# Optimization experiments

Measured on AMD Instinct MI355X. Metric: run time of the kernel, lower is better.

## Reference

```python
import jax, jax.numpy as jnp
import numpy as np

B, N, HIDDEN = 4, 2048, 512
N_HEADS, HEAD_DIM = 8, 64
N_CANCER = 32
SCALE = float(np.sqrt(HEAD_DIM))


def setup_inputs() -> dict:
    key = jax.random.key(0)
    ks = jax.random.split(key, 16)
    s = 0.02
    return {
        "x": jax.random.normal(ks[0], (B, N, HIDDEN), dtype=jnp.float32),
        "cancer_type": jax.random.randint(ks[1], (B,), 0, N_CANCER, dtype=jnp.int64),
        "attn_mask": jnp.zeros((B, N), dtype=bool),
        "wq": jax.random.normal(ks[2], (HIDDEN, HIDDEN), dtype=jnp.float32) * s,
        "bq": jnp.zeros((HIDDEN,), dtype=jnp.float32),
        "wk": jax.random.normal(ks[3], (HIDDEN, HIDDEN), dtype=jnp.float32) * s,
        "bk": jnp.zeros((HIDDEN,), dtype=jnp.float32),
        "wv": jax.random.normal(ks[4], (HIDDEN, HIDDEN), dtype=jnp.float32) * s,
        "bv": jnp.zeros((HIDDEN,), dtype=jnp.float32),
        "wo": jax.random.normal(ks[5], (HIDDEN, HIDDEN), dtype=jnp.float32) * s,
        "bo": jnp.zeros((HIDDEN,), dtype=jnp.float32),
        "bias_emb": jax.random.normal(ks[6], (N_CANCER, N_HEADS), dtype=jnp.float32) * s,
        "keymod_emb": jax.random.normal(ks[7], (N_CANCER, HIDDEN), dtype=jnp.float32) * s,
    }


def reference(x, cancer_type, attn_mask, wq, bq, wk, bk, wv, bv, wo, bo, bias_emb, keymod_emb):
    Bc, Nc, _ = x.shape
    # projections (torch Linear: x @ W.T + b), split heads -> (B, H, N, D)
    def split_heads(t):
        return t.reshape(Bc, Nc, N_HEADS, HEAD_DIM).transpose(0, 2, 1, 3)
    q = split_heads(x @ wq.T + bq)
    k = split_heads(x @ wk.T + bk)
    v = split_heads(x @ wv.T + bv)
    # cancer-conditioned key offset: (B, H, 1, D)
    ct_key = keymod_emb[cancer_type].reshape(Bc, 1, N_HEADS, HEAD_DIM).transpose(0, 2, 1, 3)
    k = k + ct_key
    # scores + per-head cancer bias
    attn = jnp.einsum("bhnd,bhmd->bhnm", q, k) / SCALE
    ct_bias = bias_emb[cancer_type]  # (B, H)
    attn = attn + ct_bias[:, :, None, None]
    attn = jnp.where(attn_mask[:, None, None, :], -jnp.inf, attn)
    attn = jax.nn.softmax(attn, axis=-1)
    # dropout is identity in eval mode
    out = jnp.einsum("bhnm,bhmd->bhnd", attn, v)
    out = out.transpose(0, 2, 1, 3).reshape(Bc, Nc, HIDDEN)
    return out @ wo.T + bo
```

## Files before the change

### kernel.cpp

```cpp
#include <hip/hip_runtime.h>

#define B_    4
#define N_    2048
#define HID   512
#define NH    8
#define HD    64
#define TOK   (B_ * N_)
#define LOG2E 1.4426950408889634f

typedef __attribute__((ext_vector_type(8))) short short8;
typedef __attribute__((ext_vector_type(4))) float f32x4;
typedef unsigned short u16;

static __device__ __forceinline__ u16 f2bf(float f) {
    unsigned int u = __builtin_bit_cast(unsigned int, f);
    u += 0x7FFFu + ((u >> 16) & 1u);
    return (u16)(u >> 16);
}
static __device__ __forceinline__ float bf2f(u16 v) {
    return __builtin_bit_cast(float, (unsigned)v << 16);
}
static __device__ __forceinline__ unsigned pktrunc(float a, float b) {
    return __builtin_amdgcn_perm(__builtin_bit_cast(unsigned, b),
                                 __builtin_bit_cast(unsigned, a), 0x07060302u);
}

static __device__ __forceinline__ void dma16(const void* g, void* l) {
    __builtin_amdgcn_global_load_lds(
        (const __attribute__((address_space(1))) unsigned int*)(unsigned long long)g,
        (__attribute__((address_space(3))) unsigned int*)(unsigned int)(unsigned long long)l,
        16, 0, 0);
}

__global__ __launch_bounds__(256) void cvt_all(
    const float* __restrict__ x,
    const float* __restrict__ w0, const float* __restrict__ w1,
    const float* __restrict__ w2, const float* __restrict__ w3,
    u16* __restrict__ xb,
    u16* __restrict__ d0, u16* __restrict__ d1,
    u16* __restrict__ d2, u16* __restrict__ d3)
{
    const int bid = blockIdx.x;
    const float* s;
    u16* d;
    int off;
    if (bid < 4096) { s = x; d = xb; off = bid; }
    else {
        const int t = (bid - 4096) >> 8;
        off = (bid - 4096) & 255;
        s = t == 0 ? w0 : t == 1 ? w1 : t == 2 ? w2 : w3;
        d = t == 0 ? d0 : t == 1 ? d1 : t == 2 ? d2 : d3;
    }
    const int i = off * 1024 + threadIdx.x * 4;
    const float4 v = *(const float4*)&s[i];
    ushort4 o;
    o.x = f2bf(v.x); o.y = f2bf(v.y); o.z = f2bf(v.z); o.w = f2bf(v.w);
    *(ushort4*)&d[i] = o;
}

__global__ __launch_bounds__(256) void gemm_qkv(
    const u16* __restrict__ xb,
    const u16* __restrict__ W0, const u16* __restrict__ W1, const u16* __restrict__ W2,
    const float* __restrict__ bias0, const float* __restrict__ bias1, const float* __restrict__ bias2,
    u16* __restrict__ Qg, u16* __restrict__ Kg, u16* __restrict__ Vtg)
{
    const int z = blockIdx.z;
    const u16*   Wz   = z == 0 ? W0 : z == 1 ? W1 : W2;
    const float* bias = z == 0 ? bias0 : z == 1 ? bias1 : bias2;

    const u16* Ap; const u16* Bp; int arow0, brow0;
    if (z < 2) { Ap = Wz; Bp = xb; arow0 = blockIdx.y * 128; brow0 = blockIdx.x * 128; }
    else       { Ap = xb; Bp = Wz; arow0 = blockIdx.x * 128; brow0 = blockIdx.y * 128; }

    __shared__ u16 ABs[2][2][128 * 32];

    const int tid  = threadIdx.x;
    const int w    = tid >> 6, lane = tid & 63;
    const int wr   = w >> 1, wc = w & 1;
    const int t16  = lane & 15, q4 = lane >> 4;

    const int dmr  = lane >> 2;
    const int dmc8 = (lane & 3) ^ ((lane >> 2) & 3) ^ ((lane >> 4) & 3);

    f32x4 acc[4][4];
    #pragma unroll
    for (int mt = 0; mt < 4; ++mt)
        #pragma unroll
        for (int nt = 0; nt < 4; ++nt)
            acc[mt][nt] = (f32x4){0.f, 0.f, 0.f, 0.f};

    #define QKV_DMA(p, k0)                                                      \
        _Pragma("unroll")                                                       \
        for (int i = 0; i < 2; ++i) {                                           \
            const int c = w * 2 + i;                                            \
            dma16(&Ap[(size_t)(arow0 + c * 16 + dmr) * HID + (k0) + dmc8 * 8],  \
                  &ABs[p][0][c * 512]);                                         \
            dma16(&Bp[(size_t)(brow0 + c * 16 + dmr) * HID + (k0) + dmc8 * 8],  \
                  &ABs[p][1][c * 512]);                                         \
        }

    QKV_DMA(0, 0)

    const int swz = (t16 ^ (t16 >> 2)) & 3;

    for (int it = 0; it < HID / 32; ++it) {
        __syncthreads();
        if (it + 1 < HID / 32) { QKV_DMA((it + 1) & 1, (it + 1) * 32) }

        const int p = it & 1;
        short8 af[4], bf[4];
        #pragma unroll
        for (int mt = 0; mt < 4; ++mt)
            af[mt] = *(const short8*)&ABs[p][0][(wr * 64 + mt * 16 + t16) * 32 + (q4 ^ swz) * 8];
        #pragma unroll
        for (int nt = 0; nt < 4; ++nt)
            bf[nt] = *(const short8*)&ABs[p][1][(wc * 64 + nt * 16 + t16) * 32 + (q4 ^ swz) * 8];
        #pragma unroll
        for (int mt = 0; mt < 4; ++mt)
            #pragma unroll
            for (int nt = 0; nt < 4; ++nt)
                acc[mt][nt] = __builtin_amdgcn_mfma_f32_16x16x32_bf16(
                    af[mt], bf[nt], acc[mt][nt], 0, 0, 0);
    }

    if (z < 2) {
        const float qs = (z == 0) ? 0.125f * LOG2E : 1.0f;
        u16* Cg = (z == 0) ? Qg : Kg;
        u16 (*St)[72] = (u16(*)[72])&ABs[0][0][0];
        #pragma unroll
        for (int p = 0; p < 2; ++p) {
            __syncthreads();
            if (wr == p) {
                #pragma unroll
                for (int mt = 0; mt < 4; ++mt) {
                    const f32x4 bv = *(const f32x4*)&bias[arow0 + p * 64 + mt * 16 + q4 * 4];
                    #pragma unroll
                    for (int nt = 0; nt < 4; ++nt) {
                        const int np = wc * 64 + nt * 16 + t16;
                        uint2 pk;
                        pk.x = pktrunc((acc[mt][nt][0] + bv[0]) * qs,
                                       (acc[mt][nt][1] + bv[1]) * qs);
                        pk.y = pktrunc((acc[mt][nt][2] + bv[2]) * qs,
                                       (acc[mt][nt][3] + bv[3]) * qs);
                        *(uint2*)&St[np][mt * 16 + q4 * 4] = pk;
                    }
                }
            }
            __syncthreads();
            const int h = blockIdx.y * 2 + p;
            #pragma unroll
            for (int it = 0; it < 4; ++it) {
                const int task = tid + it * 256;
                const int np = task >> 3, ch = task & 7;
                const int nf = brow0 + np;
                const int b = nf >> 11, n = nf & (N_ - 1);
                *(short8*)&Cg[(((size_t)(b * NH + h)) * N_ + n) * HD + ch * 8] =
                    *(const short8*)&St[np][ch * 8];
            }
        }
    } else {
        u16 (*St)[72] = (u16(*)[72])&ABs[0][0][0];
        const int b = arow0 >> 11;
        #pragma unroll
        for (int p = 0; p < 2; ++p) {
            __syncthreads();
            if (wr == p) {
                #pragma unroll
                for (int nt = 0; nt < 4; ++nt) {
                    const int jp = wc * 64 + nt * 16 + t16;
                    const float bv = bias[brow0 + jp];
                    #pragma unroll
                    for (int mt = 0; mt < 4; ++mt) {
                        uint2 pk;
                        pk.x = pktrunc(acc[mt][nt][0] + bv, acc[mt][nt][1] + bv);
                        pk.y = pktrunc(acc[mt][nt][2] + bv, acc[mt][nt][3] + bv);
                        *(uint2*)&St[jp][mt * 16 + q4 * 4] = pk;
                    }
                }
            }
            __syncthreads();
            const int nb = (arow0 & (N_ - 1)) + p * 64;
            #pragma unroll
            for (int it = 0; it < 2; ++it) {
                const int task = tid + it * 256;
                const int jp = task >> 2, qc = task & 3;
                u16 v[16];
                #pragma unroll
                for (int e = 0; e < 16; ++e) {
                    const int np = qc * 16 + e;
                    const int n  = ((np & 3) << 4) | (np >> 2);
                    v[e] = St[jp][n];
                }
                const int j = brow0 + jp, h = j >> 6, d = j & 63;
                u16* dst = &Vtg[(((size_t)(b * NH + h)) * HD + d) * N_ + nb + qc * 16];
                *(short8*)(dst)     = *(const short8*)&v[0];
                *(short8*)(dst + 8) = *(const short8*)&v[8];
            }
        }
    }
}

__global__ __launch_bounds__(256) void gemm_o(
    const u16* __restrict__ A, const u16* __restrict__ W,
    const float* __restrict__ bias, float* __restrict__ C)
{
    __shared__ u16 ABs[2][(64 + 128) * 32];

    const int tid  = threadIdx.x;
    const int row0 = blockIdx.x * 64, col0 = blockIdx.y * 128;
    const int w    = tid >> 6, lane = tid & 63;
    const int wr   = w >> 1, wc = w & 1;
    const int t16  = lane & 15, q4 = lane >> 4;

    const int dmr  = lane >> 2;
    const int dmc8 = (lane & 3) ^ ((lane >> 2) & 3) ^ ((lane >> 4) & 3);

    f32x4 acc[2][4];
    #pragma unroll
    for (int mt = 0; mt < 2; ++mt)
        #pragma unroll
        for (int nt = 0; nt < 4; ++nt)
            acc[mt][nt] = (f32x4){0.f, 0.f, 0.f, 0.f};

    #define O_DMA(p, k0)                                                        \
        dma16(&A[(size_t)(row0 + w * 16 + dmr) * HID + (k0) + dmc8 * 8],        \
              &ABs[p][w * 512]);                                                \
        _Pragma("unroll")                                                       \
        for (int i = 0; i < 2; ++i) {                                           \
            const int c = w * 2 + i;                                            \
            dma16(&W[(size_t)(col0 + c * 16 + dmr) * HID + (k0) + dmc8 * 8],    \
                  &ABs[p][2048 + c * 512]);                                     \
        }

    O_DMA(0, 0)

    const int swz = (t16 ^ (t16 >> 2)) & 3;

    for (int it = 0; it < HID / 32; ++it) {
        __syncthreads();
        if (it + 1 < HID / 32) { O_DMA((it + 1) & 1, (it + 1) * 32) }

        const int p = it & 1;
        short8 af[2], bf[4];
        #pragma unroll
        for (int mt = 0; mt < 2; ++mt)
            af[mt] = *(const short8*)&ABs[p][(wr * 32 + mt * 16 + t16) * 32 + (q4 ^ swz) * 8];
        #pragma unroll
        for (int nt = 0; nt < 4; ++nt)
            bf[nt] = *(const short8*)&ABs[p][2048 + (wc * 64 + nt * 16 + t16) * 32 + (q4 ^ swz) * 8];
        #pragma unroll
        for (int mt = 0; mt < 2; ++mt)
            #pragma unroll
            for (int nt = 0; nt < 4; ++nt)
                acc[mt][nt] = __builtin_amdgcn_mfma_f32_16x16x32_bf16(
                    af[mt], bf[nt], acc[mt][nt], 0, 0, 0);
    }

    #pragma unroll
    for (int nt = 0; nt < 4; ++nt) {
        const int j = col0 + wc * 64 + nt * 16 + t16;
        const float bv = bias[j];
        #pragma unroll
        for (int mt = 0; mt < 2; ++mt)
            #pragma unroll
            for (int r = 0; r < 4; ++r) {
                const int i = row0 + wr * 32 + mt * 16 + q4 * 4 + r;
                C[(size_t)i * HID + j] = acc[mt][nt][r] + bv;
            }
    }
}

__global__ __launch_bounds__(256) void flash_mfma(
    const u16* __restrict__ Qg, const u16* __restrict__ Kg,
    const u16* __restrict__ Vtg, const unsigned char* __restrict__ msk,
    u16* __restrict__ Op, float* __restrict__ Lp)
{
    __shared__ u16 KVs[2][2][64 * 64];
    __shared__ u16 Ps[4][32][72];
    __shared__ unsigned Mnd[16][32];

    const int tid = threadIdx.x;
    const int w = tid >> 6, lane = tid & 63;
    const int t16 = lane & 15, q4 = lane >> 4;
    const int bh = blockIdx.y, b = bh >> 3;
    const int z = blockIdx.z;
    const int kofs = z * (N_ / 2);
    const int qrow0 = blockIdx.x * 128;
    const int qbase = qrow0 + w * 32;

    const size_t hb = (size_t)bh * N_ * HD;
    const u16* Qh  = Qg + hb;
    const u16* Kh  = Kg + hb;
    const u16* Vth = Vtg + hb;
    const unsigned char* mrow = msk + b * N_;

    #pragma unroll
    for (int it = 0; it < 2; ++it) {
        const int e = tid + it * 256;
        const int kt = e >> 5, sl = e & 31;
        const int tt = sl >> 1, wd = sl & 1;
        const int k0 = kofs + kt * 64 + wd * 32 + tt;
        const unsigned lo = mrow[k0]      ? 0u : 0x0000FFFFu;
        const unsigned hi = mrow[k0 + 16] ? 0u : 0xFFFF0000u;
        Mnd[kt][sl] = lo | hi;
    }

    short8 qf[2][2];
    #pragma unroll
    for (int mt = 0; mt < 2; ++mt)
        #pragma unroll
        for (int kk = 0; kk < 2; ++kk)
            qf[mt][kk] = *(const short8*)
                &Qh[(size_t)(qbase + mt * 16 + t16) * HD + kk * 32 + q4 * 8];

    const short8 ones8 = {0x3F80, 0x3F80, 0x3F80, 0x3F80,
                          0x3F80, 0x3F80, 0x3F80, 0x3F80};

    f32x4 o[2][4], ls[2];
    #pragma unroll
    for (int mt = 0; mt < 2; ++mt) {
        #pragma unroll
        for (int nt = 0; nt < 4; ++nt) o[mt][nt] = (f32x4){0.f, 0.f, 0.f, 0.f};
        ls[mt] = (f32x4){0.f, 0.f, 0.f, 0.f};
    }

    const int dmr  = lane >> 3;
    const int dmc8 = (lane & 7) ^ ((lane >> 3) & 7);

    #define FLASH_DMA(p, kb)                                                    \
        _Pragma("unroll")                                                       \
        for (int i = 0; i < 2; ++i) {                                           \
            const int c = w * 2 + i;                                            \
            dma16(&Kh[(size_t)((kb) + c * 8 + dmr) * HD + dmc8 * 8],            \
                  &KVs[p][0][c * 512]);                                         \
            dma16(&Vth[(size_t)(c * 8 + dmr) * N_ + (kb) + dmc8 * 8],           \
                  &KVs[p][1][c * 512]);                                         \
        }

    FLASH_DMA(0, kofs)

    const int swz7 = t16 & 7;

    for (int kt = 0; kt < 16; ++kt) {
        __syncthreads();
        if (kt + 1 < 16) { FLASH_DMA((kt + 1) & 1, kofs + (kt + 1) * 64) }
        const int p = kt & 1;

        f32x4 s[2][4];
        #pragma unroll
        for (int mt = 0; mt < 2; ++mt)
            #pragma unroll
            for (int f = 0; f < 4; ++f)
                s[mt][f] = (f32x4){0.f, 0.f, 0.f, 0.f};
        #pragma unroll
        for (int f = 0; f < 4; ++f) {
            #pragma unroll
            for (int kk = 0; kk < 2; ++kk) {
                const short8 kf = *(const short8*)
                    &KVs[p][0][(f * 16 + t16) * 64 + ((kk * 4 + q4) ^ swz7) * 8];
                #pragma unroll
                for (int mt = 0; mt < 2; ++mt)
                    s[mt][f] = __builtin_amdgcn_mfma_f32_16x16x32_bf16(
                        qf[mt][kk], kf, s[mt][f], 0, 0, 0);
            }
        }

        const uint2 mnd = *(const uint2*)&Mnd[kt][t16 * 2];

        #pragma unroll
        for (int mt = 0; mt < 2; ++mt) {
            #pragma unroll
            for (int r = 0; r < 4; ++r) {
                const float e0 = __builtin_amdgcn_exp2f(s[mt][0][r]);
                const float e1 = __builtin_amdgcn_exp2f(s[mt][1][r]);
                const float e2 = __builtin_amdgcn_exp2f(s[mt][2][r]);
                const float e3 = __builtin_amdgcn_exp2f(s[mt][3][r]);
                uint2 pk;
                pk.x = pktrunc(e0, e1) & mnd.x;
                pk.y = pktrunc(e2, e3) & mnd.y;
                *(uint2*)&Ps[w][mt * 16 + q4 * 4 + r][t16 * 4] = pk;
            }
        }

        short8 pf[2][2];
        #pragma unroll
        for (int mt = 0; mt < 2; ++mt)
            #pragma unroll
            for (int kk = 0; kk < 2; ++kk)
                pf[mt][kk] = *(const short8*)&Ps[w][mt * 16 + t16][kk * 32 + q4 * 8];
        #pragma unroll
        for (int mt = 0; mt < 2; ++mt)
            #pragma unroll
            for (int kk = 0; kk < 2; ++kk)
                ls[mt] = __builtin_amdgcn_mfma_f32_16x16x32_bf16(
                    pf[mt][kk], ones8, ls[mt], 0, 0, 0);
        #pragma unroll
        for (int nt = 0; nt < 4; ++nt) {
            #pragma unroll
            for (int kk = 0; kk < 2; ++kk) {
                const short8 vf = *(const short8*)
                    &KVs[p][1][(nt * 16 + t16) * 64 + ((kk * 4 + q4) ^ swz7) * 8];
                #pragma unroll
                for (int mt = 0; mt < 2; ++mt)
                    o[mt][nt] = __builtin_amdgcn_mfma_f32_16x16x32_bf16(
                        pf[mt][kk], vf, o[mt][nt], 0, 0, 0);
            }
        }
    }

    const size_t obase = (((size_t)z * 32 + bh)) * N_ * HD;
    #pragma unroll
    for (int mt = 0; mt < 2; ++mt) {
        #pragma unroll
        for (int r = 0; r < 4; ++r) {
            const int n = qbase + mt * 16 + q4 * 4 + r;
            if (t16 == 0) Lp[((size_t)z * 32 + bh) * N_ + n] = ls[mt][r];
            #pragma unroll
            for (int nt = 0; nt < 4; ++nt)
                Op[obase + (size_t)n * HD + nt * 16 + t16] = f2bf(o[mt][nt][r]);
        }
    }
}

__global__ __launch_bounds__(256) void reduce_o(
    const u16* __restrict__ Op, const float* __restrict__ Lp,
    u16* __restrict__ AOg)
{
    const int e = blockIdx.x * 256 + threadIdx.x;
    const int d4 = e & 15;
    const int n  = (e >> 4) & (N_ - 1);
    const int bh = e >> 15;
    const size_t base = (((size_t)bh) * N_ + n) * HD + d4 * 4;
    const ushort4 a = *(const ushort4*)&Op[base];
    const ushort4 c = *(const ushort4*)&Op[(size_t)32 * N_ * HD + base];
    const float inv = 1.f / (Lp[(size_t)bh * N_ + n] + Lp[(size_t)(32 + bh) * N_ + n]);
    ushort4 o;
    o.x = f2bf((bf2f(a.x) + bf2f(c.x)) * inv);
    o.y = f2bf((bf2f(a.y) + bf2f(c.y)) * inv);
    o.z = f2bf((bf2f(a.z) + bf2f(c.z)) * inv);
    o.w = f2bf((bf2f(a.w) + bf2f(c.w)) * inv);
    const int b = bh >> 3, h = bh & 7;
    *(ushort4*)&AOg[(((size_t)b * N_ + n)) * HID + h * 64 + d4 * 4] = o;
}

extern "C" void kernel_launch(void* const* d_in, const int* in_sizes, int n_in,
                              void* d_out, int out_size, void* d_ws, size_t ws_size,
                              hipStream_t stream) {
    const float* x  = (const float*)d_in[0];
    const unsigned char* mask = (const unsigned char*)d_in[2];
    const float* wq = (const float*)d_in[3];
    const float* bq = (const float*)d_in[4];
    const float* wk = (const float*)d_in[5];
    const float* bk = (const float*)d_in[6];
    const float* wv = (const float*)d_in[7];
    const float* bv = (const float*)d_in[8];
    const float* wo = (const float*)d_in[9];
    const float* bo = (const float*)d_in[10];

    char* ws = (char*)d_ws;
    u16* xb  = (u16*)(ws);
    u16* wqb = (u16*)(ws + (8u << 20));
    u16* wkb = (u16*)(ws + (8u << 20) + (512u << 10));
    u16* wvb = (u16*)(ws + (8u << 20) + (1024u << 10));
    u16* wob = (u16*)(ws + (8u << 20) + (1536u << 10));
    u16* Qg  = (u16*)(ws + (10u << 20));
    u16* Kg  = (u16*)(ws + (18u << 20));
    u16* Vtg = (u16*)(ws + (26u << 20));
    u16* Op  = (u16*)(ws + (34u << 20));
    float* Lp = (float*)(ws + (50u << 20));
    u16* AOg = xb;

    cvt_all<<<5120, 256, 0, stream>>>(x, wq, wk, wv, wo, xb, wqb, wkb, wvb, wob);

    gemm_qkv<<<dim3(TOK / 128, HID / 128, 3), 256, 0, stream>>>(
        xb, wqb, wkb, wvb, bq, bk, bv, Qg, Kg, Vtg);

    flash_mfma<<<dim3(N_ / 128, B_ * NH, 2), 256, 0, stream>>>(
        Qg, Kg, Vtg, mask, Op, Lp);

    reduce_o<<<(32 * N_ * 16) / 256, 256, 0, stream>>>(Op, Lp, AOg);

    gemm_o<<<dim3(TOK / 64, HID / 128), 256, 0, stream>>>(
        AOg, wob, bo, (float*)d_out);
}
```

Baseline: 179.3 us.

## Fuse split-softmax reduction into output projection GEMM and unroll double-buffer loops

Removes the separate reduce_o kernel and instead has the output-projection GEMM load both flash-attention partial outputs plus their row sums, combine and normalise them, and stage the bf16 result into shared memory as the A operand. This drops one launch and one full round trip of the attention output through global memory. The new GEMM uses smaller 32-row tiles with only half the threads doing the A loads, which may reduce MFMA efficiency. The QKV GEMM and flash loops are also unrolled by two so the ping-pong buffer index is a compile-time constant.

```diff
diff --git a/kernel.cpp b/kernel.cpp
--- a/kernel.cpp
+++ b/kernel.cpp
@@ -99,15 +99,9 @@
                   &ABs[p][1][c * 512]);                                         \
         }
 
-    QKV_DMA(0, 0)
-
     const int swz = (t16 ^ (t16 >> 2)) & 3;
 
-    for (int it = 0; it < HID / 32; ++it) {
-        __syncthreads();
-        if (it + 1 < HID / 32) { QKV_DMA((it + 1) & 1, (it + 1) * 32) }
-
-        const int p = it & 1;
+    auto qstep = [&](const int p) {
         short8 af[4], bf[4];
         #pragma unroll
         for (int mt = 0; mt < 4; ++mt)
@@ -121,6 +115,16 @@
             for (int nt = 0; nt < 4; ++nt)
                 acc[mt][nt] = __builtin_amdgcn_mfma_f32_16x16x32_bf16(
                     af[mt], bf[nt], acc[mt][nt], 0, 0, 0);
+    };
+
+    QKV_DMA(0, 0)
+    for (int it = 0; it < 16; it += 2) {
+        __syncthreads();
+        QKV_DMA(1, (it + 1) * 32)
+        qstep(0);
+        __syncthreads();
+        if (it + 2 < 16) { QKV_DMA(0, (it + 2) * 32) }
+        qstep(1);
     }
 
     if (z < 2) {
@@ -200,76 +204,6 @@
     }
 }
 
-__global__ __launch_bounds__(256) void gemm_o(
-    const u16* __restrict__ A, const u16* __restrict__ W,
-    const float* __restrict__ bias, float* __restrict__ C)
-{
-    __shared__ u16 ABs[2][(64 + 128) * 32];
-
-    const int tid  = threadIdx.x;
-    const int row0 = blockIdx.x * 64, col0 = blockIdx.y * 128;
-    const int w    = tid >> 6, lane = tid & 63;
-    const int wr   = w >> 1, wc = w & 1;
-    const int t16  = lane & 15, q4 = lane >> 4;
-
-    const int dmr  = lane >> 2;
-    const int dmc8 = (lane & 3) ^ ((lane >> 2) & 3) ^ ((lane >> 4) & 3);
-
-    f32x4 acc[2][4];
-    #pragma unroll
-    for (int mt = 0; mt < 2; ++mt)
-        #pragma unroll
-        for (int nt = 0; nt < 4; ++nt)
-            acc[mt][nt] = (f32x4){0.f, 0.f, 0.f, 0.f};
-
-    #define O_DMA(p, k0)                                                        \
-        dma16(&A[(size_t)(row0 + w * 16 + dmr) * HID + (k0) + dmc8 * 8],        \
-              &ABs[p][w * 512]);                                                \
-        _Pragma("unroll")                                                       \
-        for (int i = 0; i < 2; ++i) {                                           \
-            const int c = w * 2 + i;                                            \
-            dma16(&W[(size_t)(col0 + c * 16 + dmr) * HID + (k0) + dmc8 * 8],    \
-                  &ABs[p][2048 + c * 512]);                                     \
-        }
-
-    O_DMA(0, 0)
-
-    const int swz = (t16 ^ (t16 >> 2)) & 3;
-
-    for (int it = 0; it < HID / 32; ++it) {
-        __syncthreads();
-        if (it + 1 < HID / 32) { O_DMA((it + 1) & 1, (it + 1) * 32) }
-
-        const int p = it & 1;
-        short8 af[2], bf[4];
-        #pragma unroll
-        for (int mt = 0; mt < 2; ++mt)
-            af[mt] = *(const short8*)&ABs[p][(wr * 32 + mt * 16 + t16) * 32 + (q4 ^ swz) * 8];
-        #pragma unroll
-        for (int nt = 0; nt < 4; ++nt)
-            bf[nt] = *(const short8*)&ABs[p][2048 + (wc * 64 + nt * 16 + t16) * 32 + (q4 ^ swz) * 8];
-        #pragma unroll
-        for (int mt = 0; mt < 2; ++mt)
-            #pragma unroll
-            for (int nt = 0; nt < 4; ++nt)
-                acc[mt][nt] = __builtin_amdgcn_mfma_f32_16x16x32_bf16(
-                    af[mt], bf[nt], acc[mt][nt], 0, 0, 0);
-    }
-
-    #pragma unroll
-    for (int nt = 0; nt < 4; ++nt) {
-        const int j = col0 + wc * 64 + nt * 16 + t16;
-        const float bv = bias[j];
-        #pragma unroll
-        for (int mt = 0; mt < 2; ++mt)
-            #pragma unroll
-            for (int r = 0; r < 4; ++r) {
-                const int i = row0 + wr * 32 + mt * 16 + q4 * 4 + r;
-                C[(size_t)i * HID + j] = acc[mt][nt][r] + bv;
-            }
-    }
-}
-
 __global__ __launch_bounds__(256) void flash_mfma(
     const u16* __restrict__ Qg, const u16* __restrict__ Kg,
     const u16* __restrict__ Vtg, const unsigned char* __restrict__ msk,
@@ -337,15 +271,9 @@
                   &KVs[p][1][c * 512]);                                         \
         }
 
-    FLASH_DMA(0, kofs)
-
     const int swz7 = t16 & 7;
 
-    for (int kt = 0; kt < 16; ++kt) {
-        __syncthreads();
-        if (kt + 1 < 16) { FLASH_DMA((kt + 1) & 1, kofs + (kt + 1) * 64) }
-        const int p = kt & 1;
-
+    auto fstep = [&](const int p, const int kt) {
         f32x4 s[2][4];
         #pragma unroll
         for (int mt = 0; mt < 2; ++mt)
@@ -406,6 +334,16 @@
                         pf[mt][kk], vf, o[mt][nt], 0, 0, 0);
             }
         }
+    };
+
+    FLASH_DMA(0, kofs)
+    for (int kt = 0; kt < 16; kt += 2) {
+        __syncthreads();
+        FLASH_DMA(1, kofs + (kt + 1) * 64)
+        fstep(0, kt);
+        __syncthreads();
+        if (kt + 2 < 16) { FLASH_DMA(0, kofs + (kt + 2) * 64) }
+        fstep(1, kt + 1);
     }
 
     const size_t obase = (((size_t)z * 32 + bh)) * N_ * HD;
@@ -422,25 +360,98 @@
     }
 }
 
-__global__ __launch_bounds__(256) void reduce_o(
+__global__ __launch_bounds__(256) void gemm_o2(
     const u16* __restrict__ Op, const float* __restrict__ Lp,
-    u16* __restrict__ AOg)
+    const u16* __restrict__ W, const float* __restrict__ bias,
+    float* __restrict__ C)
 {
-    const int e = blockIdx.x * 256 + threadIdx.x;
-    const int d4 = e & 15;
-    const int n  = (e >> 4) & (N_ - 1);
-    const int bh = e >> 15;
-    const size_t base = (((size_t)bh) * N_ + n) * HD + d4 * 4;
-    const ushort4 a = *(const ushort4*)&Op[base];
-    const ushort4 c = *(const ushort4*)&Op[(size_t)32 * N_ * HD + base];
-    const float inv = 1.f / (Lp[(size_t)bh * N_ + n] + Lp[(size_t)(32 + bh) * N_ + n]);
-    ushort4 o;
-    o.x = f2bf((bf2f(a.x) + bf2f(c.x)) * inv);
-    o.y = f2bf((bf2f(a.y) + bf2f(c.y)) * inv);
-    o.z = f2bf((bf2f(a.z) + bf2f(c.z)) * inv);
-    o.w = f2bf((bf2f(a.w) + bf2f(c.w)) * inv);
-    const int b = bh >> 3, h = bh & 7;
-    *(ushort4*)&AOg[(((size_t)b * N_ + n)) * HID + h * 64 + d4 * 4] = o;
+    __shared__ u16 As[2][32][40];
+    __shared__ u16 Bs[2][128 * 32];
+
+    const int tid  = threadIdx.x;
+    const int row0 = blockIdx.x * 32, col0 = blockIdx.y * 128;
+    const int w    = tid >> 6, lane = tid & 63;
+    const int wr   = w >> 1, wc = w & 1;
+    const int t16  = lane & 15, q4 = lane >> 4;
+
+    const int dmr  = lane >> 2;
+    const int dmc8 = (lane & 3) ^ ((lane >> 2) & 3) ^ ((lane >> 4) & 3);
+
+    f32x4 acc[4];
+    #pragma unroll
+    for (int nt = 0; nt < 4; ++nt) acc[nt] = (f32x4){0.f, 0.f, 0.f, 0.f};
+
+    #define O2_DMA(p, k0)                                                       \
+        _Pragma("unroll")                                                       \
+        for (int i = 0; i < 2; ++i) {                                           \
+            const int c = w * 2 + i;                                            \
+            dma16(&W[(size_t)(col0 + c * 16 + dmr) * HID + (k0) + dmc8 * 8],    \
+                  &Bs[p][c * 512]);                                             \
+        }
+
+    const int tr = tid >> 2, dcol = (tid & 3) * 8;
+    const int itok = row0 + tr;
+    const int ab = itok >> 11, an = itok & (N_ - 1);
+    short8 a0, a1;
+    float inv;
+    const size_t OP_HALF = (size_t)32 * N_ * HD;
+
+    auto aload = [&](const int t) {
+        const int h = t >> 1, dk = (t & 1) * 32;
+        const size_t li  = ((size_t)(ab * NH + h)) * N_ + an;
+        const size_t off = li * HD + dk + dcol;
+        a0 = *(const short8*)&Op[off];
+        a1 = *(const short8*)&Op[off + OP_HALF];
+        inv = 1.f / (Lp[li] + Lp[li + (size_t)32 * N_]);
+    };
+
+    const int swz = (t16 ^ (t16 >> 2)) & 3;
+
+    auto ostep = [&](const int p, const int t) {
+        if (tid < 128) {
+            float v[8];
+            #pragma unroll
+            for (int i = 0; i < 8; ++i)
+                v[i] = (bf2f((u16)a0[i]) + bf2f((u16)a1[i])) * inv;
+            uint4 pk;
+            pk.x = pktrunc(v[0], v[1]);
+            pk.y = pktrunc(v[2], v[3]);
+            pk.z = pktrunc(v[4], v[5]);
+            pk.w = pktrunc(v[6], v[7]);
+            *(uint4*)&As[p][tr][dcol] = pk;
+        }
+        __syncthreads();
+        if (t + 1 < 16) {
+            O2_DMA(p ^ 1, (t + 1) * 32)
+            if (tid < 128) aload(t + 1);
+        }
+        const short8 af = *(const short8*)&As[p][wr * 16 + t16][q4 * 8];
+        short8 bf[4];
+        #pragma unroll
+        for (int nt = 0; nt < 4; ++nt)
+            bf[nt] = *(const short8*)&Bs[p][(wc * 64 + nt * 16 + t16) * 32 + (q4 ^ swz) * 8];
+        #pragma unroll
+        for (int nt = 0; nt < 4; ++nt)
+            acc[nt] = __builtin_amdgcn_mfma_f32_16x16x32_bf16(af, bf[nt], acc[nt], 0, 0, 0);
+    };
+
+    O2_DMA(0, 0)
+    if (tid < 128) aload(0);
+    for (int t = 0; t < 16; t += 2) {
+        ostep(0, t);
+        ostep(1, t + 1);
+    }
+
+    #pragma unroll
+    for (int nt = 0; nt < 4; ++nt) {
+        const int j = col0 + wc * 64 + nt * 16 + t16;
+        const float bv = bias[j];
+        #pragma unroll
+        for (int r = 0; r < 4; ++r) {
+            const int i = row0 + wr * 16 + q4 * 4 + r;
+            C[(size_t)i * HID + j] = acc[nt][r] + bv;
+        }
+    }
 }
 
 extern "C" void kernel_launch(void* const* d_in, const int* in_sizes, int n_in,
@@ -468,7 +479,6 @@
     u16* Vtg = (u16*)(ws + (26u << 20));
     u16* Op  = (u16*)(ws + (34u << 20));
     float* Lp = (float*)(ws + (50u << 20));
-    u16* AOg = xb;
 
     cvt_all<<<5120, 256, 0, stream>>>(x, wq, wk, wv, wo, xb, wqb, wkb, wvb, wob);
 
@@ -478,8 +488,6 @@
     flash_mfma<<<dim3(N_ / 128, B_ * NH, 2), 256, 0, stream>>>(
         Qg, Kg, Vtg, mask, Op, Lp);
 
-    reduce_o<<<(32 * N_ * 16) / 256, 256, 0, stream>>>(Op, Lp, AOg);
-
-    gemm_o<<<dim3(TOK / 64, HID / 128), 256, 0, stream>>>(
-        AOg, wob, bo, (float*)d_out);
-}
+    gemm_o2<<<dim3(TOK / 32, HID / 128), 256, 0, stream>>>(
+        Op, Lp, wob, bo, (float*)d_out);
+}
```

After: 178.8 us. About the same (-0.3%).
